# Kernel optimization log

Measured on AMD Instinct MI355X. Metric: run time of the kernel, lower is better.

Reference implementation:

```python
import jax, jax.numpy as jnp
import numpy as np

N_CELLS = 1000          # cells in minibatch
N_GENES_OI = 500        # genes in minibatch
N_GENES_TOTAL = 5000    # fragments.n_genes
N_LATENT = 10           # latent (cluster) dim
NBINS = 128             # quadratic spline bins
N_KNOTS = NBINS + 1     # knot heights = mixture delta components
N_CUTS = 1_000_000      # fragment cut sites (ragged dim)


def setup_inputs() -> dict:
    key = jax.random.key(0)
    ks = jax.random.split(key, 10)
    return {
        "latent": jax.random.normal(ks[0], (N_CELLS, N_LATENT), jnp.float32),
        "cut_coordinates": jax.random.uniform(ks[1], (N_CUTS,), jnp.float32),
        "genes_oi": jax.random.randint(ks[2], (N_GENES_OI,), 0, N_GENES_TOTAL),
        "cut_local_cellxgene_ix": jax.random.randint(ks[3], (N_CUTS,), 0, N_CELLS * N_GENES_OI),
        "cut_localcellxgene_ix": jax.random.randint(ks[4], (N_CUTS,), 0, N_CELLS * N_GENES_TOTAL),
        "cut_local_gene_ix": jax.random.randint(ks[5], (N_CUTS,), 0, N_GENES_OI),
        "height_slope_w": jax.random.normal(ks[6], (N_GENES_TOTAL, N_LATENT, N_KNOTS), jnp.float32) * 0.1,
        "overall_slope_w": jax.random.normal(ks[7], (N_GENES_TOTAL, N_LATENT), jnp.float32) * 0.1,
        "overall_baseline": jax.random.normal(ks[8], (N_GENES_TOTAL,), jnp.float32),
        "spline_baseline": jax.random.normal(ks[9], (N_GENES_TOTAL, N_KNOTS), jnp.float32) * 0.5,
    }


def quadratic_spline_log_prob(x, heights):
    """Piecewise-linear density (quadratic CDF spline) with K equal-width bins.
    heights: [ncuts, K+1] unnormalized log knot heights; x in [0,1]."""
    K = heights.shape[-1] - 1
    h = heights - jnp.max(heights, axis=-1, keepdims=True)  # stable; pdf invariant to shift
    u = jnp.exp(h)
    # trapezoid integral with width 1/K
    norm = jnp.sum(0.5 * (u[:, :-1] + u[:, 1:]), axis=-1) / K
    pdf = u / norm[:, None]                                 # [ncuts, K+1]
    xs = jnp.clip(x, 0.0, 1.0 - 1e-6) * K
    b = jnp.clip(jnp.floor(xs).astype(jnp.int32), 0, K - 1)  # bin index
    alpha = xs - b
    left = jnp.take_along_axis(pdf, b[:, None], axis=1)[:, 0]
    right = jnp.take_along_axis(pdf, (b + 1)[:, None], axis=1)[:, 0]
    return jnp.log(left + alpha * (right - left))


def reference(latent, cut_coordinates, genes_oi, cut_local_cellxgene_ix,
              cut_localcellxgene_ix, cut_local_gene_ix, height_slope_w,
              overall_slope_w, overall_baseline, spline_baseline):
    # decoder: per-gene slope embeddings modulated by cell latent
    height_delta = jnp.einsum('cl,glk->cgk', latent, height_slope_w[genes_oi])  # [N, Goi, K+1]
    overall_delta = latent @ overall_slope_w.T                                  # [N, G]
    # softmax over all genes -> per cell x gene overall rate
    overall_cellxgene = jax.nn.softmax(overall_baseline[None, :] + overall_delta, axis=-1)
    # ragged gathers per cut
    overall = overall_cellxgene.reshape(-1)[cut_localcellxgene_ix]              # [ncuts]
    height = height_delta.reshape(-1, height_delta.shape[-1])[cut_local_cellxgene_ix]  # [ncuts, K+1]
    gene_per_cut = genes_oi[cut_local_gene_ix]
    heights = spline_baseline[gene_per_cut] + height                            # [ncuts, K+1]
    likelihood_height = quadratic_spline_log_prob(cut_coordinates, heights)
    likelihood = likelihood_height + jnp.log(overall) + jnp.log(jnp.float32(N_GENES_TOTAL))
    elbo = -jnp.sum(likelihood)
    return elbo
```

## Files before the change

### kernel.cpp

```cpp
#include <hip/hip_runtime.h>
#include <hip/hip_fp16.h>

#define N_CELLS   1000
#define N_GOI     500
#define N_GTOT    5000
#define N_LAT     10
#define NBINS     128
#define N_KNOTS   129
#define LOG_NGT   8.517193191416238f
#define LOG_NBINS 4.852030263919617f
#define LSE_CPB   4
#define OVB       20
#define CUTS_PT   2

typedef int   vint2   __attribute__((ext_vector_type(2)));
typedef float vfloat2 __attribute__((ext_vector_type(2)));

#if defined(__has_builtin)
#if __has_builtin(__builtin_amdgcn_cvt_pk_f32_fp8) && \
    __has_builtin(__builtin_amdgcn_cvt_pk_fp8_f32)
#define HW_FP8 1
#endif
#endif

#ifdef HW_FP8
#define DEC2(w, hi) ((vfloat2)__builtin_amdgcn_cvt_pk_f32_fp8((int)(w), (hi)))
__device__ __forceinline__ unsigned enc1(float x) {
    return (unsigned)__builtin_amdgcn_cvt_pk_fp8_f32(x, x, 0, false) & 0xffu;
}
#else
__device__ __forceinline__ float dec1_sw(unsigned b) {
    unsigned s = b >> 7, e = (b >> 3) & 15, m = b & 7;
    float v = (e == 0) ? ldexpf((float)m, -9)
                       : ldexpf((float)(8 + m), (int)e - 10);
    return s ? -v : v;
}
__device__ __forceinline__ vfloat2 dec2_sw(unsigned w, int hi) {
    unsigned sh = hi ? 16u : 0u;
    vfloat2 r;
    r.x = dec1_sw((w >> sh) & 0xffu);
    r.y = dec1_sw((w >> (sh + 8)) & 0xffu);
    return r;
}
#define DEC2(w, hi) dec2_sw((w), (hi))
__device__ __forceinline__ unsigned enc1(float x) {
    unsigned s = (__float_as_uint(x) >> 31) << 7;
    float ax = fabsf(x);
    if (!(ax > 0.0f)) return s;
    ax = fminf(ax, 448.0f);
    int e; frexpf(ax, &e);
    int qe = (e - 1 < -6) ? -9 : e - 4;
    float rq = ldexpf(rintf(ldexpf(ax, -qe)), qe);
    if (rq == 0.0f) return s;
    frexpf(rq, &e);
    int be = e - 1 + 7;
    if (be <= 0) return s | (unsigned)rintf(ldexpf(rq, 9));
    unsigned mm = (unsigned)rintf(ldexpf(rq, -(e - 1)) * 8.0f);
    return s | ((unsigned)be << 3) | (mm - 8u);
}
#endif

__device__ __forceinline__ float2 upk(unsigned u) {
    union { unsigned u; __half2 h; } cv; cv.u = u;
    return __half22float2(cv.h);
}
__device__ __forceinline__ __half2 h2u(unsigned u) {
    union { unsigned u; __half2 h; } cv; cv.u = u;
    return cv.h;
}
__device__ __forceinline__ float dec1(unsigned b) { return DEC2(b, false).x; }


__global__ __launch_bounds__(256) void prep_pair_kernel(
    const float* __restrict__ latent,
    const float* __restrict__ osw,
    const float* __restrict__ ob,
    const int*  __restrict__ genes_oi,
    const float* __restrict__ hsw,
    const float* __restrict__ sbase,
    __half* __restrict__ latA,
    __half* __restrict__ latB,
    uint4*  __restrict__ wpair,
    uint4*  __restrict__ ovp8,
    signed char* __restrict__ lnsq,
    float* __restrict__ out)
{
    const int t = threadIdx.x;
    __shared__ uint4          wdup4[N_KNOTS * 3];
    __shared__ unsigned char  bq[N_KNOTS * 10];
    __shared__ unsigned short hq[N_KNOTS];
    __shared__ float          wred[4][LSE_CPB];

    if (blockIdx.x < N_GOI) {
        const int gi = blockIdx.x;
        const int g  = genes_oi[gi];
        {
            unsigned* wd = (unsigned*)wdup4;
            for (int e = t; e < N_KNOTS * 12; e += 256) {
                const int k = e / 12;
                const int l = e - 12 * k;
                unsigned dup = 0u;
                if (l < N_LAT) {
                    const unsigned b8 = enc1(hsw[(g * N_LAT + l) * N_KNOTS + k]);
                    bq[k * 10 + l] = (unsigned char)b8;
                    const unsigned hb =
                        (unsigned)__half_as_ushort(__float2half(dec1(b8)));
                    dup = hb | (hb << 16);
                } else if (l == N_LAT) {
                    const __half h = __float2half(sbase[g * N_KNOTS + k]);
                    hq[k] = __half_as_ushort(h);
                    const unsigned hb = (unsigned)__half_as_ushort(h);
                    dup = hb | (hb << 16);
                }
                wd[e] = dup;
            }
        }
        __syncthreads();

        {
            const int b   = t >> 1;
            const int hf  = t & 1;
            const int row = b + hf;
            const unsigned char* bb = bq + row * 10;
            uint4 rec;
            rec.x = (unsigned)bb[0] | ((unsigned)bb[1] << 8) |
                    ((unsigned)bb[2] << 16) | ((unsigned)bb[3] << 24);
            rec.y = (unsigned)bb[4] | ((unsigned)bb[5] << 8) |
                    ((unsigned)bb[6] << 16) | ((unsigned)bb[7] << 24);
            rec.z = (unsigned)bb[8] | ((unsigned)bb[9] << 8) |
                    ((unsigned)hq[row] << 16);
            rec.w = 0u;
            wpair[(gi * 128 + b) * 2 + hf] = rec;
        }

        __half2 lA[N_LAT], lB[N_LAT];
        {
            const int cA0 = t;
            const int cA1 = t + 256;
            const int cB0 = t + 512;
            const int cB1 = (t + 768 < N_CELLS) ? t + 768 : 0;
#pragma unroll
            for (int l = 0; l < N_LAT; ++l) {
                lA[l] = __halves2half2(__float2half(latent[cA0 * N_LAT + l]),
                                       __float2half(latent[cA1 * N_LAT + l]));
                lB[l] = __halves2half2(__float2half(latent[cB0 * N_LAT + l]),
                                       __float2half(latent[cB1 * N_LAT + l]));
            }
        }

        float s0 = 0.f, s1 = 0.f, s2 = 0.f, s3 = 0.f;
#pragma unroll 2
        for (int k = 0; k <= NBINS; ++k) {
            const float tw = (k == 0 || k == NBINS) ? 0.5f : 1.0f;
            const uint4 a = wdup4[k * 3];
            const uint4 b = wdup4[k * 3 + 1];
            const uint4 c = wdup4[k * 3 + 2];
            __half2 dA = h2u(c.z), dB = h2u(c.z);
            dA = __hfma2(lA[0], h2u(a.x), dA); dB = __hfma2(lB[0], h2u(a.x), dB);
            dA = __hfma2(lA[1], h2u(a.y), dA); dB = __hfma2(lB[1], h2u(a.y), dB);
            dA = __hfma2(lA[2], h2u(a.z), dA); dB = __hfma2(lB[2], h2u(a.z), dB);
            dA = __hfma2(lA[3], h2u(a.w), dA); dB = __hfma2(lB[3], h2u(a.w), dB);
            dA = __hfma2(lA[4], h2u(b.x), dA); dB = __hfma2(lB[4], h2u(b.x), dB);
            dA = __hfma2(lA[5], h2u(b.y), dA); dB = __hfma2(lB[5], h2u(b.y), dB);
            dA = __hfma2(lA[6], h2u(b.z), dA); dB = __hfma2(lB[6], h2u(b.z), dB);
            dA = __hfma2(lA[7], h2u(b.w), dA); dB = __hfma2(lB[7], h2u(b.w), dB);
            dA = __hfma2(lA[8], h2u(c.x), dA); dB = __hfma2(lB[8], h2u(c.x), dB);
            dA = __hfma2(lA[9], h2u(c.y), dA); dB = __hfma2(lB[9], h2u(c.y), dB);
            const float2 fA = __half22float2(dA);
            const float2 fB = __half22float2(dB);
            s0 += tw * __expf(fA.x);
            s1 += tw * __expf(fA.y);
            s2 += tw * __expf(fB.x);
            s3 += tw * __expf(fB.y);
        }
        {
            float sums[4] = {s0, s1, s2, s3};
#pragma unroll
            for (int j = 0; j < 4; ++j) {
                const int c = t + j * 256;
                if (c < N_CELLS) {
                    const float lns = __logf(sums[j]) - LOG_NBINS;
                    const float qv = fminf(fmaxf(lns * 32.0f, -127.0f), 127.0f);
                    lnsq[gi * N_CELLS + c] = (signed char)(int)rintf(qv);
                }
            }
        }
    } else if (blockIdx.x < N_GOI + N_CELLS / LSE_CPB) {
        const int cb = (blockIdx.x - N_GOI) * LSE_CPB;
        float lat[LSE_CPB][N_LAT];
#pragma unroll
        for (int j = 0; j < LSE_CPB; ++j) {
            const float2* l2 = (const float2*)(latent + (cb + j) * N_LAT);
#pragma unroll
            for (int h = 0; h < 5; ++h) {
                const float2 v2 = l2[h];
                lat[j][2 * h]     = v2.x;
                lat[j][2 * h + 1] = v2.y;
            }
        }
        float s[LSE_CPB] = {0.f, 0.f, 0.f, 0.f};
        for (int g = t; g < N_GTOT; g += 256) {
            const float bb = ob[g];
            const float2* o2 = (const float2*)(osw + g * N_LAT);
            float2 w0 = o2[0], w1 = o2[1], w2 = o2[2], w3 = o2[3], w4 = o2[4];
#pragma unroll
            for (int j = 0; j < LSE_CPB; ++j) {
                float v = bb;
                v = fmaf(lat[j][0], w0.x, v); v = fmaf(lat[j][1], w0.y, v);
                v = fmaf(lat[j][2], w1.x, v); v = fmaf(lat[j][3], w1.y, v);
                v = fmaf(lat[j][4], w2.x, v); v = fmaf(lat[j][5], w2.y, v);
                v = fmaf(lat[j][6], w3.x, v); v = fmaf(lat[j][7], w3.y, v);
                v = fmaf(lat[j][8], w4.x, v); v = fmaf(lat[j][9], w4.y, v);
                s[j] += __expf(v);
            }
        }
#pragma unroll
        for (int j = 0; j < LSE_CPB; ++j)
#pragma unroll
            for (int off = 32; off; off >>= 1) s[j] += __shfl_xor(s[j], off);
        if ((t & 63) == 0)
#pragma unroll
            for (int j = 0; j < LSE_CPB; ++j) wred[t >> 6][j] = s[j];
        __syncthreads();
        if (t < 12 * LSE_CPB) {
            const int j = t / 12;
            const int l = t - 12 * j;
            const float bias = LOG_NGT -
                __logf(wred[0][j] + wred[1][j] + wred[2][j] + wred[3][j]);
            const int c = cb + j;
            if (l < 8) {
                latA[c * 8 + l] = __float2half(latent[c * N_LAT + l]);
            } else {
                float v;
                if (l < N_LAT)       v = latent[c * N_LAT + l];
                else if (l == N_LAT) v = 1.0f;
                else                 v = bias;
                latB[c * 4 + (l - 8)] = __float2half(v);
            }
        }
    } else {
        const int vb = blockIdx.x - N_GOI - N_CELLS / LSE_CPB;
        for (int g = vb * 256 + t; g < N_GTOT; g += OVB * 256) {
            const float* o = osw + g * N_LAT;
            uint4 rec;
            rec.x = enc1(o[0]) | (enc1(o[1]) << 8) |
                    (enc1(o[2]) << 16) | (enc1(o[3]) << 24);
            rec.y = enc1(o[4]) | (enc1(o[5]) << 8) |
                    (enc1(o[6]) << 16) | (enc1(o[7]) << 24);
            rec.z = enc1(o[8]) | (enc1(o[9]) << 8) |
                    ((unsigned)__half_as_ushort(__float2half(ob[g])) << 16);
            rec.w = 0u;
            ovp8[g] = rec;
        }
        if (vb == 0 && t == 0) *out = 0.0f;
    }
}

__device__ __forceinline__ float cut_term(
    int pi, int qi, float x,
    const __half* __restrict__ lshA,
    const __half* __restrict__ lshB,
    const uint4*  __restrict__ wpair,
    const uint4*  __restrict__ ovp8,
    const signed char* __restrict__ lnsq)
{
    const unsigned p    = (unsigned)pi;
    const unsigned cell = p / (unsigned)N_GOI;
    const unsigned gl   = p - cell * (unsigned)N_GOI;
    const unsigned q    = (unsigned)qi;
    const unsigned c2   = q / (unsigned)N_GTOT;
    const unsigned g2   = q - c2 * (unsigned)N_GTOT;

    float xs = fminf(fmaxf(x, 0.0f), 1.0f - 1e-6f) * (float)NBINS;
    int b = (int)xs;
    b = b < NBINS - 1 ? b : NBINS - 1;
    const float alpha = xs - (float)b;

    const uint4 r0 = wpair[((gl << 7) + b) * 2];
    const uint4 r1 = wpair[((gl << 7) + b) * 2 + 1];
    const uint4 ov = ovp8[g2];
    const float lns = (float)lnsq[gl * (unsigned)N_CELLS + cell] * 0.03125f;

    const uint4 lca = *(const uint4*)(lshA + (cell << 3));
    const uint2 lcb = *(const uint2*)(lshB + (cell << 2));
    const uint4 mca = *(const uint4*)(lshA + (c2 << 3));
    const uint2 mcb = *(const uint2*)(lshB + (c2 << 2));

    const float2 a0 = upk(lca.x), a1 = upk(lca.y), a2 = upk(lca.z),
                 a3 = upk(lca.w), a4 = upk(lcb.x);

    vfloat2 w01 = DEC2(r0.x, false), w23 = DEC2(r0.x, true),
            w45 = DEC2(r0.y, false), w67 = DEC2(r0.y, true),
            w89 = DEC2(r0.z, false);
    float d0 = upk(r0.z).y;
    d0 = fmaf(a0.x, w01.x, d0); d0 = fmaf(a0.y, w01.y, d0);
    d0 = fmaf(a1.x, w23.x, d0); d0 = fmaf(a1.y, w23.y, d0);
    d0 = fmaf(a2.x, w45.x, d0); d0 = fmaf(a2.y, w45.y, d0);
    d0 = fmaf(a3.x, w67.x, d0); d0 = fmaf(a3.y, w67.y, d0);
    d0 = fmaf(a4.x, w89.x, d0); d0 = fmaf(a4.y, w89.y, d0);

    vfloat2 v01 = DEC2(r1.x, false), v23 = DEC2(r1.x, true),
            v45 = DEC2(r1.y, false), v67 = DEC2(r1.y, true),
            v89 = DEC2(r1.z, false);
    float d1 = upk(r1.z).y;
    d1 = fmaf(a0.x, v01.x, d1); d1 = fmaf(a0.y, v01.y, d1);
    d1 = fmaf(a1.x, v23.x, d1); d1 = fmaf(a1.y, v23.y, d1);
    d1 = fmaf(a2.x, v45.x, d1); d1 = fmaf(a2.y, v45.y, d1);
    d1 = fmaf(a3.x, v67.x, d1); d1 = fmaf(a3.y, v67.y, d1);
    d1 = fmaf(a4.x, v89.x, d1); d1 = fmaf(a4.y, v89.y, d1);

    const float ul = __expf(d0);
    const float ur = __expf(d1);
    const float pv = fmaf(alpha, ur - ul, ul);

    const float2 m0 = upk(mca.x), m1 = upk(mca.y), m2 = upk(mca.z),
                 m3 = upk(mca.w), m4 = upk(mcb.x), mb = upk(mcb.y);
    vfloat2 o01 = DEC2(ov.x, false), o23 = DEC2(ov.x, true),
            o45 = DEC2(ov.y, false), o67 = DEC2(ov.y, true),
            o89 = DEC2(ov.z, false);
    float dv = upk(ov.z).y + mb.y;
    dv = fmaf(m0.x, o01.x, dv); dv = fmaf(m0.y, o01.y, dv);
    dv = fmaf(m1.x, o23.x, dv); dv = fmaf(m1.y, o23.y, dv);
    dv = fmaf(m2.x, o45.x, dv); dv = fmaf(m2.y, o45.y, dv);
    dv = fmaf(m3.x, o67.x, dv); dv = fmaf(m3.y, o67.y, dv);
    dv = fmaf(m4.x, o89.x, dv); dv = fmaf(m4.y, o89.y, dv);

    return __logf(pv) - lns + dv;
}

__global__ __launch_bounds__(256) void cut_kernel(
    const __half* __restrict__ latA,
    const __half* __restrict__ latB,
    const uint4*  __restrict__ wpair,
    const uint4*  __restrict__ ovp8,
    const signed char* __restrict__ lnsq,
    const float* __restrict__ coords,
    const int*  __restrict__ cxg,
    const int*  __restrict__ cxgtot,
    float* __restrict__ out, int n)
{
    const int t = threadIdx.x;
    __shared__ __half lshA[N_CELLS * 8];
    __shared__ __half lshB[N_CELLS * 4];
    {
        const uint4* sA = (const uint4*)latA;
        uint4* dA = (uint4*)lshA;
        for (int e = t; e < (N_CELLS * 8) / 8; e += 256) dA[e] = sA[e];
        const uint4* sB = (const uint4*)latB;
        uint4* dB = (uint4*)lshB;
        for (int e = t; e < (N_CELLS * 4) / 8; e += 256) dB[e] = sB[e];
    }
    __syncthreads();

    double acc = 0.0;
    const int i0 = (blockIdx.x * 256 + t) * CUTS_PT;
    if (i0 + CUTS_PT - 1 < n) {
        const vint2   P = __builtin_nontemporal_load((const vint2*)(cxg + i0));
        const vint2   Q = __builtin_nontemporal_load((const vint2*)(cxgtot + i0));
        const vfloat2 X = __builtin_nontemporal_load((const vfloat2*)(coords + i0));
        acc += (double)cut_term(P.x, Q.x, X.x, lshA, lshB, wpair, ovp8, lnsq);
        acc += (double)cut_term(P.y, Q.y, X.y, lshA, lshB, wpair, ovp8, lnsq);
    } else if (i0 < n) {
        for (int i = i0; i < n; ++i)
            acc += (double)cut_term(cxg[i], cxgtot[i], coords[i],
                                    lshA, lshB, wpair, ovp8, lnsq);
    }

#pragma unroll
    for (int off = 32; off; off >>= 1) acc += __shfl_xor(acc, off);
    __shared__ double part[4];
    if ((t & 63) == 0) part[t >> 6] = acc;
    __syncthreads();
    if (t == 0)
        atomicAdd(out, (float)(-(part[0] + part[1] + part[2] + part[3])));
}

extern "C" void kernel_launch(void* const* d_in, const int* in_sizes, int n_in,
                              void* d_out, int out_size, void* d_ws, size_t ws_size,
                              hipStream_t stream)
{
    const float* latent   = (const float*)d_in[0];
    const float* coords   = (const float*)d_in[1];
    const int*   genes_oi = (const int*)  d_in[2];
    const int*   cxg      = (const int*)  d_in[3];
    const int*   cxg_tot  = (const int*)  d_in[4];
    const float* hsw      = (const float*)d_in[6];
    const float* osw      = (const float*)d_in[7];
    const float* ob       = (const float*)d_in[8];
    const float* sbase    = (const float*)d_in[9];
    const int ncuts = in_sizes[1];

    char* ws = (char*)d_ws;
    __half* latA  = (__half*)(ws);
    __half* latB  = (__half*)(ws + 16000);
    uint4*  wpair = (uint4*) (ws + 24000);
    uint4*  ovp8  = (uint4*) (ws + 2072000);
    signed char* lnsq = (signed char*)(ws + 2152000);
    float*  out   = (float*)d_out;

    prep_pair_kernel<<<N_GOI + N_CELLS / LSE_CPB + OVB, 256, 0, stream>>>(
        latent, osw, ob, genes_oi, hsw, sbase,
        latA, latB, wpair, ovp8, lnsq, out);

    const int nq = (ncuts + CUTS_PT - 1) / CUTS_PT;
    const int blocks = (nq + 255) >> 8;
    cut_kernel<<<blocks, 256, 0, stream>>>(
        latA, latB, wpair, ovp8, lnsq, coords, cxg, cxg_tot, out, ncuts);
}
```

Baseline: 156.0 us.

## Store knot rows once per gene and process four cuts per thread

Changes the per-gene packed weight table from duplicated bin pairs (two 16-byte records per bin) to a single row per knot, read as two adjacent records. This halves the table size (about 2 MB down to about 1 MB), which improves cache residency for the random gathers. Each cut-kernel thread now handles four cuts with 16-byte vector loads instead of two. That cuts block count and the per-block shared-memory latent staging, in exchange for more registers per thread and fewer waves.

```diff
diff --git a/kernel.cpp b/kernel.cpp
--- a/kernel.cpp
+++ b/kernel.cpp
@@ -11,9 +11,10 @@
 #define LOG_NBINS 4.852030263919617f
 #define LSE_CPB   4
 #define OVB       20
-#define CUTS_PT   2
-
-typedef int   vint2   __attribute__((ext_vector_type(2)));
+#define CUTS_PT   4
+
+typedef int   vint4   __attribute__((ext_vector_type(4)));
+typedef float vfloat4 __attribute__((ext_vector_type(4)));
 typedef float vfloat2 __attribute__((ext_vector_type(2)));
 
 #if defined(__has_builtin)
@@ -80,7 +81,7 @@
     const float* __restrict__ sbase,
     __half* __restrict__ latA,
     __half* __restrict__ latB,
-    uint4*  __restrict__ wpair,
+    uint4*  __restrict__ wrow,
     uint4*  __restrict__ ovp8,
     signed char* __restrict__ lnsq,
     float* __restrict__ out)
@@ -117,20 +118,17 @@
         }
         __syncthreads();
 
-        {
-            const int b   = t >> 1;
-            const int hf  = t & 1;
-            const int row = b + hf;
-            const unsigned char* bb = bq + row * 10;
+        if (t < N_KNOTS) {
+            const unsigned char* bb = bq + t * 10;
             uint4 rec;
             rec.x = (unsigned)bb[0] | ((unsigned)bb[1] << 8) |
                     ((unsigned)bb[2] << 16) | ((unsigned)bb[3] << 24);
             rec.y = (unsigned)bb[4] | ((unsigned)bb[5] << 8) |
                     ((unsigned)bb[6] << 16) | ((unsigned)bb[7] << 24);
             rec.z = (unsigned)bb[8] | ((unsigned)bb[9] << 8) |
-                    ((unsigned)hq[row] << 16);
+                    ((unsigned)hq[t] << 16);
             rec.w = 0u;
-            wpair[(gi * 128 + b) * 2 + hf] = rec;
+            wrow[gi * N_KNOTS + t] = rec;
         }
 
         __half2 lA[N_LAT], lB[N_LAT];
@@ -260,7 +258,7 @@
     int pi, int qi, float x,
     const __half* __restrict__ lshA,
     const __half* __restrict__ lshB,
-    const uint4*  __restrict__ wpair,
+    const uint4*  __restrict__ wrow,
     const uint4*  __restrict__ ovp8,
     const signed char* __restrict__ lnsq)
 {
@@ -276,8 +274,9 @@
     b = b < NBINS - 1 ? b : NBINS - 1;
     const float alpha = xs - (float)b;
 
-    const uint4 r0 = wpair[((gl << 7) + b) * 2];
-    const uint4 r1 = wpair[((gl << 7) + b) * 2 + 1];
+    const uint4* rp = wrow + (gl * N_KNOTS + b);
+    const uint4 r0 = rp[0];
+    const uint4 r1 = rp[1];
     const uint4 ov = ovp8[g2];
     const float lns = (float)lnsq[gl * (unsigned)N_CELLS + cell] * 0.03125f;
 
@@ -331,7 +330,7 @@
 __global__ __launch_bounds__(256) void cut_kernel(
     const __half* __restrict__ latA,
     const __half* __restrict__ latB,
-    const uint4*  __restrict__ wpair,
+    const uint4*  __restrict__ wrow,
     const uint4*  __restrict__ ovp8,
     const signed char* __restrict__ lnsq,
     const float* __restrict__ coords,
@@ -355,15 +354,17 @@
     double acc = 0.0;
     const int i0 = (blockIdx.x * 256 + t) * CUTS_PT;
     if (i0 + CUTS_PT - 1 < n) {
-        const vint2   P = __builtin_nontemporal_load((const vint2*)(cxg + i0));
-        const vint2   Q = __builtin_nontemporal_load((const vint2*)(cxgtot + i0));
-        const vfloat2 X = __builtin_nontemporal_load((const vfloat2*)(coords + i0));
-        acc += (double)cut_term(P.x, Q.x, X.x, lshA, lshB, wpair, ovp8, lnsq);
-        acc += (double)cut_term(P.y, Q.y, X.y, lshA, lshB, wpair, ovp8, lnsq);
+        const vint4   P = __builtin_nontemporal_load((const vint4*)(cxg + i0));
+        const vint4   Q = __builtin_nontemporal_load((const vint4*)(cxgtot + i0));
+        const vfloat4 X = __builtin_nontemporal_load((const vfloat4*)(coords + i0));
+        acc += (double)cut_term(P.x, Q.x, X.x, lshA, lshB, wrow, ovp8, lnsq);
+        acc += (double)cut_term(P.y, Q.y, X.y, lshA, lshB, wrow, ovp8, lnsq);
+        acc += (double)cut_term(P.z, Q.z, X.z, lshA, lshB, wrow, ovp8, lnsq);
+        acc += (double)cut_term(P.w, Q.w, X.w, lshA, lshB, wrow, ovp8, lnsq);
     } else if (i0 < n) {
         for (int i = i0; i < n; ++i)
             acc += (double)cut_term(cxg[i], cxgtot[i], coords[i],
-                                    lshA, lshB, wpair, ovp8, lnsq);
+                                    lshA, lshB, wrow, ovp8, lnsq);
     }
 
 #pragma unroll
@@ -393,17 +394,17 @@
     char* ws = (char*)d_ws;
     __half* latA  = (__half*)(ws);
     __half* latB  = (__half*)(ws + 16000);
-    uint4*  wpair = (uint4*) (ws + 24000);
-    uint4*  ovp8  = (uint4*) (ws + 2072000);
-    signed char* lnsq = (signed char*)(ws + 2152000);
+    uint4*  wrow  = (uint4*) (ws + 24000);
+    uint4*  ovp8  = (uint4*) (ws + 1056000);
+    signed char* lnsq = (signed char*)(ws + 1136000);
     float*  out   = (float*)d_out;
 
     prep_pair_kernel<<<N_GOI + N_CELLS / LSE_CPB + OVB, 256, 0, stream>>>(
         latent, osw, ob, genes_oi, hsw, sbase,
-        latA, latB, wpair, ovp8, lnsq, out);
+        latA, latB, wrow, ovp8, lnsq, out);
 
     const int nq = (ncuts + CUTS_PT - 1) / CUTS_PT;
     const int blocks = (nq + 255) >> 8;
     cut_kernel<<<blocks, 256, 0, stream>>>(
-        latA, latB, wpair, ovp8, lnsq, coords, cxg, cxg_tot, out, ncuts);
-}
+        latA, latB, wrow, ovp8, lnsq, coords, cxg, cxg_tot, out, ncuts);
+}
```

Result: faster. 150.8 us (-3.3%).
